# Optimization experiments

Hardware: AMD Instinct MI355X
Metric: run time of the kernel (lower is better)

## Reference

```python
import jax, jax.numpy as jnp
import numpy as np

B, ENC_IN, ENC_HID, N, GH = 64, 64, 256, 2048, 128
LN_EPS = 1e-5


def _chain_adjacency(n):
    # tridiagonal chain adjacency, D^{-1/2} A D^{-1/2} normalized
    off = jnp.ones((n - 1,), dtype=jnp.float32)
    A = jnp.diag(off, 1) + jnp.diag(off, -1)
    deg = A.sum(axis=1)
    d_inv_sqrt = jnp.power(deg + 1e-8, -0.5)
    return A * d_inv_sqrt[None, :] * d_inv_sqrt[:, None]


def setup_inputs() -> dict:
    key = jax.random.key(0)
    ks = jax.random.split(key, 16)
    s = 0.02
    return {
        "x": jax.random.normal(ks[0], (B, ENC_IN), dtype=jnp.float32),
        "A_hat": _chain_adjacency(N),
        "W1": jax.random.normal(ks[1], (ENC_IN, ENC_HID), dtype=jnp.float32) * s,
        "b1": jnp.zeros((ENC_HID,), dtype=jnp.float32),
        "W2": jax.random.normal(ks[2], (ENC_HID, N * GH), dtype=jnp.float32) * s,
        "b2": jnp.zeros((N * GH,), dtype=jnp.float32),
        "Wg1": jax.random.normal(ks[3], (GH, GH), dtype=jnp.float32) * s,
        "Wg2": jax.random.normal(ks[4], (GH, GH), dtype=jnp.float32) * s,
        "ln_g1": jnp.ones((GH,), dtype=jnp.float32),
        "ln_b1": jnp.zeros((GH,), dtype=jnp.float32),
        "ln_g2": jnp.ones((GH,), dtype=jnp.float32),
        "ln_b2": jnp.zeros((GH,), dtype=jnp.float32),
        "Wout": jax.random.normal(ks[5], (GH, 1), dtype=jnp.float32) * s,
        "bout": jnp.zeros((1,), dtype=jnp.float32),
    }


def _layernorm(h, g, b):
    mu = h.mean(axis=-1, keepdims=True)
    var = ((h - mu) ** 2).mean(axis=-1, keepdims=True)
    return (h - mu) * jax.lax.rsqrt(var + LN_EPS) * g + b


def reference(x, A_hat, W1, b1, W2, b2, Wg1, Wg2, ln_g1, ln_b1, ln_g2, ln_b2, Wout, bout):
    # encoder MLP -> (B, N, GH) node features
    enc = jax.nn.relu(x @ W1 + b1) @ W2 + b2
    out = enc.reshape(B, N, GH)
    # GCN layers: out = out + A_hat @ (LN(out) W)   (dropout is identity at eval)
    for Wg, g, bb in ((Wg1, ln_g1, ln_b1), (Wg2, ln_g2, ln_b2)):
        h = _layernorm(out, g, bb)
        Wx = h @ Wg                              # (B, N, GH)
        out = out + jnp.einsum('ij,bjd->bid', A_hat, Wx)
    return (out @ Wout + bout).squeeze(-1)       # (B, N)
```

## Files before the change

kernel.cpp:

```cpp
#include <hip/hip_runtime.h>


#define B_    64
#define EIN   64
#define EHID  256
#define NN    2048
#define GH    128
#define NG    (NN*GH)
#define LN_EPS 1e-5f
#define C3    28

typedef _Float16 f16;
typedef _Float16 f16x8 __attribute__((ext_vector_type(8)));
typedef _Float16 f16x4 __attribute__((ext_vector_type(4)));
typedef _Float16 f16x2 __attribute__((ext_vector_type(2)));
typedef float    f32x4 __attribute__((ext_vector_type(4)));
typedef unsigned int u32;

#define AS1 __attribute__((address_space(1)))
#define AS3 __attribute__((address_space(3)))

__device__ __forceinline__ float wred64(float v) {
#pragma unroll
    for (int off = 32; off > 0; off >>= 1) v += __shfl_xor(v, off, 64);
    return v;
}

__global__ __launch_bounds__(256) void k_prep(
    const float* __restrict__ x,  const float* __restrict__ W1, const float* __restrict__ b1,
    const float* __restrict__ Wg1,const float* __restrict__ Wg2,const float* __restrict__ Wout,
    const float* __restrict__ A_hat,
    const float* __restrict__ ln_g2, const float* __restrict__ ln_b2,
    f16* __restrict__ h1h, f16* __restrict__ wg1T,
    float* __restrict__ u2, float* __restrict__ sc,
    float* __restrict__ clo, float* __restrict__ chi)
{
    int bid = blockIdx.x, tid = threadIdx.x;
    if (bid < 64) {
        int b = bid, j = tid;
        float acc = b1[j];
#pragma unroll 8
        for (int k = 0; k < EIN; ++k) acc = fmaf(x[b*EIN + k], W1[k*EHID + j], acc);
        h1h[b*EHID + j] = (f16)fmaxf(acc, 0.f);
    } else if (bid == 64) {
        __shared__ float tu[GH], tb[GH];
        if (tid < GH) {
            float s = 0.f;
            for (int j = 0; j < GH; ++j) s = fmaf(Wg2[tid*GH + j], Wout[j], s);
            float uu = ln_g2[tid] * s;
            u2[tid] = uu;
            tu[tid] = uu;
            tb[tid] = ln_b2[tid] * s;
        }
        __syncthreads();
        if (tid < 64) {
            float a = tu[tid] + tu[tid + 64];
            float b = tb[tid] + tb[tid + 64];
            a = wred64(a); b = wred64(b);
            if (tid == 0) { sc[0] = a; sc[1] = b; }
        }
    } else if (bid == 65) {
        for (int i = tid; i < GH*GH; i += 256) {
            int n = i >> 7, k = i & 127;
            wg1T[i] = (f16)Wg1[k*GH + n];
        }
    } else {
        int n = (bid - 66) * 256 + tid;
        clo[n] = (n >= 1)    ? A_hat[(size_t)n*NN + (n-1)] : 0.f;
        chi[n] = (n <= NN-2) ? A_hat[(size_t)n*NN + (n+1)] : 0.f;
    }
}

__global__ __launch_bounds__(256) void k_enc(
    const float* __restrict__ W2, const float* __restrict__ b2,
    const f16* __restrict__ h1h, f16* __restrict__ out0)
{
    __shared__ float w2s[2][16*516];

    int tid = threadIdx.x;
    int L = tid & 63, wv = tid >> 6, hi = L >> 4, lo = L & 15;
    int c0 = blockIdx.x * 256;

    auto stage = [&](int kk, int nb) {
#pragma unroll
        for (int s = 0; s < 8; ++s) {
            int r = wv*8 + s;
            const float* gp = W2 + (size_t)(kk*32 + r) * NG + c0 + L*4;
            float* ldst = &w2s[nb][(r >> 1)*516 + (r & 1)*256];
            __builtin_amdgcn_global_load_lds((const AS1 void*)gp, (AS3 void*)ldst, 16, 0, 0);
        }
    };

    f16x8 afq[2][4];
    auto load_af = [&](int kk, int pb) {
#pragma unroll
        for (int bg = 0; bg < 4; ++bg)
            afq[pb][bg] = *(const f16x8*)(h1h + ((bg*16 + lo) << 8) + kk*32 + hi*8);
    };

    load_af(0, 0);
    asm volatile("" ::: "memory");
    stage(0, 0);
    stage(1, 1);

    f32x4 acc[4][4];
#pragma unroll
    for (int bg = 0; bg < 4; ++bg)
#pragma unroll
        for (int t = 0; t < 4; ++t) acc[bg][t] = f32x4{0.f, 0.f, 0.f, 0.f};

#pragma unroll
    for (int kk = 0; kk < 8; ++kk) {
        if (kk < 7) asm volatile("s_waitcnt vmcnt(8)" ::: "memory");
        else        asm volatile("s_waitcnt vmcnt(0)" ::: "memory");
        __builtin_amdgcn_s_barrier();
        asm volatile("" ::: "memory");

        if (kk < 7) load_af(kk + 1, (kk + 1) & 1);

        const float* wb = w2s[kk & 1];
        f16x8 bf[4];
#pragma unroll
        for (int t = 0; t < 4; ++t)
#pragma unroll
            for (int j = 0; j < 8; ++j) {
                int row = hi*8 + j;
                bf[t][j] = (f16)wb[(row >> 1)*516 + (row & 1)*256 + wv*64 + t*16 + lo];
            }

#pragma unroll
        for (int bg = 0; bg < 4; ++bg)
#pragma unroll
            for (int t = 0; t < 4; ++t)
                acc[bg][t] = __builtin_amdgcn_mfma_f32_16x16x32_f16(afq[kk & 1][bg], bf[t], acc[bg][t], 0, 0, 0);

        asm volatile("" ::: "memory");
        __builtin_amdgcn_s_barrier();
        asm volatile("" ::: "memory");
        if (kk < 6) stage(kk + 2, kk & 1);
    }

    float bv[4];
#pragma unroll
    for (int t = 0; t < 4; ++t) bv[t] = b2[c0 + wv*64 + t*16 + lo];
#pragma unroll
    for (int bg = 0; bg < 4; ++bg)
#pragma unroll
        for (int t = 0; t < 4; ++t)
#pragma unroll
            for (int r = 0; r < 4; ++r) {
                int brow = bg*16 + hi*4 + r;
                out0[(size_t)brow * NG + c0 + wv*64 + t*16 + lo] = (f16)(acc[bg][t][r] + bv[t]);
            }
}

__global__ __launch_bounds__(256) void k_gcn(
    const float* __restrict__ clo, const float* __restrict__ chi,
    const float* __restrict__ ln_g1, const float* __restrict__ ln_b1,
    const float* __restrict__ Wout, const float* __restrict__ bout,
    const float* __restrict__ u2, const float* __restrict__ sc,
    const f16* __restrict__ wg1T,
    const f16* __restrict__ out0, float* __restrict__ y)
{
    __shared__ f16 out0_s[32][136];
    __shared__ f16 h0s[32][136];
    __shared__ f16 wx0_s[32][136];
    __shared__ alignas(16) float g1s[GH], b1s[GH], u2s[GH], wos[GH];
    __shared__ float cls[32], chs[32];
    __shared__ float ss[32], yrs[32], scs[2];

    int tid = threadIdx.x;
    int n0 = blockIdx.x * C3;
    int b  = blockIdx.y;

    for (int i = tid; i < 32*16; i += 256) {
        int r = i >> 4, gv = i & 15;
        int n = n0 - 2 + r;
        f16x8 v = {0,0,0,0,0,0,0,0};
        if (n >= 0 && n < NN) v = *(const f16x8*)(out0 + ((size_t)b*NN + n)*GH + gv*8);
        *(f16x8*)&out0_s[r][gv*8] = v;
    }
    if (tid < GH) {
        g1s[tid] = ln_g1[tid]; b1s[tid] = ln_b1[tid];
        u2s[tid] = u2[tid];    wos[tid] = Wout[tid];
    } else if (tid < GH + 32) {
        int r = tid - GH, n = n0 - 2 + r;
        bool ok = (n >= 0 && n < NN);
        cls[r] = ok ? clo[n] : 0.f;
        chs[r] = ok ? chi[n] : 0.f;
    } else if (tid == GH + 32) {
        scs[0] = sc[0]; scs[1] = sc[1];
    }
    __syncthreads();

    int L = tid & 63, wv = tid >> 6, hi = L >> 4, lo = L & 15;

    {
        f32x4 g1a = *(const f32x4*)&g1s[lo*8],     b1a = *(const f32x4*)&b1s[lo*8];
        f32x4 g1b = *(const f32x4*)&g1s[lo*8 + 4], b1b = *(const f32x4*)&b1s[lo*8 + 4];
#pragma unroll
        for (int p = 0; p < 2; ++p) {
            int r = wv*4 + hi + p*16;
            f16x8 xv = *(const f16x8*)&out0_s[r][lo*8];
            float xf[8];
#pragma unroll
            for (int c2 = 0; c2 < 8; ++c2) xf[c2] = (float)xv[c2];
            float s = 0.f, qq = 0.f;
#pragma unroll
            for (int c2 = 0; c2 < 8; ++c2) { s += xf[c2]; qq += xf[c2]*xf[c2]; }
#pragma unroll
            for (int off = 8; off > 0; off >>= 1) {
                s  += __shfl_xor(s,  off, 64);
                qq += __shfl_xor(qq, off, 64);
            }
            float mu  = s * (1.f/128.f);
            float inv = rsqrtf(qq*(1.f/128.f) - mu*mu + LN_EPS);
            f16x8 h;
            h[0] = (f16)((xf[0] - mu)*inv*g1a[0] + b1a[0]);
            h[1] = (f16)((xf[1] - mu)*inv*g1a[1] + b1a[1]);
            h[2] = (f16)((xf[2] - mu)*inv*g1a[2] + b1a[2]);
            h[3] = (f16)((xf[3] - mu)*inv*g1a[3] + b1a[3]);
            h[4] = (f16)((xf[4] - mu)*inv*g1b[0] + b1b[0]);
            h[5] = (f16)((xf[5] - mu)*inv*g1b[1] + b1b[1]);
            h[6] = (f16)((xf[6] - mu)*inv*g1b[2] + b1b[2]);
            h[7] = (f16)((xf[7] - mu)*inv*g1b[3] + b1b[3]);
            *(f16x8*)&h0s[r][lo*8] = h;
        }
    }
    __syncthreads();

    f32x4 acc[2][2];
#pragma unroll
    for (int mg = 0; mg < 2; ++mg)
#pragma unroll
        for (int nt = 0; nt < 2; ++nt) acc[mg][nt] = f32x4{0.f, 0.f, 0.f, 0.f};

#pragma unroll
    for (int kk = 0; kk < 4; ++kk) {
        f16x8 af[2], bfr[2];
#pragma unroll
        for (int mg = 0; mg < 2; ++mg)
            af[mg] = *(const f16x8*)&h0s[mg*16 + lo][kk*32 + hi*8];
#pragma unroll
        for (int nt = 0; nt < 2; ++nt) {
            int n = wv*32 + nt*16 + lo;
            bfr[nt] = *(const f16x8*)(wg1T + n*GH + kk*32 + hi*8);
        }
#pragma unroll
        for (int mg = 0; mg < 2; ++mg)
#pragma unroll
            for (int nt = 0; nt < 2; ++nt)
                acc[mg][nt] = __builtin_amdgcn_mfma_f32_16x16x32_f16(af[mg], bfr[nt], acc[mg][nt], 0, 0, 0);
    }
#pragma unroll
    for (int mg = 0; mg < 2; ++mg)
#pragma unroll
        for (int nt = 0; nt < 2; ++nt)
#pragma unroll
            for (int r = 0; r < 4; ++r)
                wx0_s[mg*16 + hi*4 + r][wv*32 + nt*16 + lo] = (f16)acc[mg][nt][r];
    __syncthreads();

    {
        f32x4 u2a = *(const f32x4*)&u2s[lo*8],     woa = *(const f32x4*)&wos[lo*8];
        f32x4 u2b = *(const f32x4*)&u2s[lo*8 + 4], wob = *(const f32x4*)&wos[lo*8 + 4];
        float S1v = scs[0], S0v = scs[1];
#pragma unroll
        for (int p = 0; p < 2; ++p) {
            int r  = wv*4 + hi + p*16;
            int rm = (r >= 1)  ? r - 1 : 0;
            int rp = (r <= 30) ? r + 1 : 31;
            float c_lo = cls[r], c_hi = chs[r];
            f16x8 ov = *(const f16x8*)&out0_s[r][lo*8];
            f16x8 av = *(const f16x8*)&wx0_s[rm][lo*8];
            f16x8 cv = *(const f16x8*)&wx0_s[rp][lo*8];
            float s = 0.f, qq = 0.f, d = 0.f, yp = 0.f;
#pragma unroll
            for (int c2 = 0; c2 < 8; ++c2) {
                float xx = (float)ov[c2] + c_lo*(float)av[c2] + c_hi*(float)cv[c2];
                float uc = (c2 < 4) ? u2a[c2] : u2b[c2-4];
                float wc = (c2 < 4) ? woa[c2] : wob[c2-4];
                s += xx; qq += xx*xx; d += xx*uc; yp += xx*wc;
            }
#pragma unroll
            for (int off = 8; off > 0; off >>= 1) {
                s  += __shfl_xor(s,  off, 64);
                qq += __shfl_xor(qq, off, 64);
                d  += __shfl_xor(d,  off, 64);
                yp += __shfl_xor(yp, off, 64);
            }
            if (lo == 0 && r >= 1 && r <= 30) {
                float mu  = s * (1.f/128.f);
                float inv = rsqrtf(qq*(1.f/128.f) - mu*mu + LN_EPS);
                ss[r]  = inv*(d - mu*S1v) + S0v;
                yrs[r] = yp;
            }
        }
    }
    __syncthreads();

    if (tid < C3) {
        int n = n0 + tid;
        if (n < NN) {
            int r = tid + 2;
            y[(size_t)b*NN + n] = yrs[r] + bout[0] + cls[r]*ss[r-1] + chs[r]*ss[r+1];
        }
    }
}

extern "C" void kernel_launch(void* const* d_in, const int* in_sizes, int n_in,
                              void* d_out, int out_size, void* d_ws, size_t ws_size,
                              hipStream_t stream)
{
    (void)in_sizes; (void)n_in; (void)out_size; (void)ws_size;
    const float* x    = (const float*)d_in[0];
    const float* A_hat= (const float*)d_in[1];
    const float* W1   = (const float*)d_in[2];
    const float* b1   = (const float*)d_in[3];
    const float* W2   = (const float*)d_in[4];
    const float* b2   = (const float*)d_in[5];
    const float* Wg1  = (const float*)d_in[6];
    const float* Wg2  = (const float*)d_in[7];
    const float* g1   = (const float*)d_in[8];
    const float* lb1  = (const float*)d_in[9];
    const float* g2   = (const float*)d_in[10];
    const float* lb2  = (const float*)d_in[11];
    const float* Wout = (const float*)d_in[12];
    const float* bout = (const float*)d_in[13];
    float* y = (float*)d_out;

    char* ws = (char*)d_ws;
    f16*   h1h  = (f16*)(ws + 0);
    f16*   wg1T = (f16*)(ws + 32768);
    float* u2   = (float*)(ws + 65536);
    float* sc   = (float*)(ws + 66560);
    float* clo  = (float*)(ws + 81920);
    float* chi  = (float*)(ws + 90112);
    f16*   out0 = (f16*)(ws + (1u << 20));

    k_prep<<<dim3(74),                   256, 0, stream>>>(x, W1, b1, Wg1, Wg2, Wout, A_hat,
                                                           g2, lb2,
                                                           h1h, wg1T, u2, sc, clo, chi);
    k_enc <<<dim3(NG/256),               256, 0, stream>>>(W2, b2, h1h, out0);
    k_gcn <<<dim3((NN + C3 - 1)/C3, B_), 256, 0, stream>>>(clo, chi, g1, lb1,
                                                           Wout, bout, u2, sc, wg1T, out0, y);
}
```

Baseline: 440.1 us.

## Keep GCN rows in registers, share one LDS tile, simplify W2 GEMM pipeline

```diff
diff --git a/kernel.cpp b/kernel.cpp
--- a/kernel.cpp
+++ b/kernel.cpp
@@ -91,17 +91,7 @@
         }
     };
 
-    f16x8 afq[2][4];
-    auto load_af = [&](int kk, int pb) {
-#pragma unroll
-        for (int bg = 0; bg < 4; ++bg)
-            afq[pb][bg] = *(const f16x8*)(h1h + ((bg*16 + lo) << 8) + kk*32 + hi*8);
-    };
-
-    load_af(0, 0);
-    asm volatile("" ::: "memory");
     stage(0, 0);
-    stage(1, 1);
 
     f32x4 acc[4][4];
 #pragma unroll
@@ -111,12 +101,8 @@
 
 #pragma unroll
     for (int kk = 0; kk < 8; ++kk) {
-        if (kk < 7) asm volatile("s_waitcnt vmcnt(8)" ::: "memory");
-        else        asm volatile("s_waitcnt vmcnt(0)" ::: "memory");
-        __builtin_amdgcn_s_barrier();
-        asm volatile("" ::: "memory");
-
-        if (kk < 7) load_af(kk + 1, (kk + 1) & 1);
+        __syncthreads();
+        if (kk < 7) stage(kk + 1, (kk + 1) & 1);
 
         const float* wb = w2s[kk & 1];
         f16x8 bf[4];
@@ -128,16 +114,16 @@
                 bf[t][j] = (f16)wb[(row >> 1)*516 + (row & 1)*256 + wv*64 + t*16 + lo];
             }
 
+        f16x8 af[4];
 #pragma unroll
         for (int bg = 0; bg < 4; ++bg)
+            af[bg] = *(const f16x8*)(h1h + ((bg*16 + lo) << 8) + kk*32 + hi*8);
+
+#pragma unroll
+        for (int bg = 0; bg < 4; ++bg)
 #pragma unroll
             for (int t = 0; t < 4; ++t)
-                acc[bg][t] = __builtin_amdgcn_mfma_f32_16x16x32_f16(afq[kk & 1][bg], bf[t], acc[bg][t], 0, 0, 0);
-
-        asm volatile("" ::: "memory");
-        __builtin_amdgcn_s_barrier();
-        asm volatile("" ::: "memory");
-        if (kk < 6) stage(kk + 2, kk & 1);
+                acc[bg][t] = __builtin_amdgcn_mfma_f32_16x16x32_f16(af[bg], bf[t], acc[bg][t], 0, 0, 0);
     }
 
     float bv[4];
@@ -162,9 +148,7 @@
     const f16* __restrict__ wg1T,
     const f16* __restrict__ out0, float* __restrict__ y)
 {
-    __shared__ f16 out0_s[32][136];
-    __shared__ f16 h0s[32][136];
-    __shared__ f16 wx0_s[32][136];
+    __shared__ f16 hw_s[32][136];
     __shared__ alignas(16) float g1s[GH], b1s[GH], u2s[GH], wos[GH];
     __shared__ float cls[32], chs[32];
     __shared__ float ss[32], yrs[32], scs[2];
@@ -172,14 +156,19 @@
     int tid = threadIdx.x;
     int n0 = blockIdx.x * C3;
     int b  = blockIdx.y;
-
-    for (int i = tid; i < 32*16; i += 256) {
-        int r = i >> 4, gv = i & 15;
+    int L = tid & 63, wv = tid >> 6, hi = L >> 4, lo = L & 15;
+
+    float xf[2][8];
+#pragma unroll
+    for (int p = 0; p < 2; ++p) {
+        int r = wv*4 + hi + p*16;
         int n = n0 - 2 + r;
         f16x8 v = {0,0,0,0,0,0,0,0};
-        if (n >= 0 && n < NN) v = *(const f16x8*)(out0 + ((size_t)b*NN + n)*GH + gv*8);
-        *(f16x8*)&out0_s[r][gv*8] = v;
-    }
+        if (n >= 0 && n < NN) v = *(const f16x8*)(out0 + ((size_t)b*NN + n)*GH + lo*8);
+#pragma unroll
+        for (int c2 = 0; c2 < 8; ++c2) xf[p][c2] = (float)v[c2];
+    }
+
     if (tid < GH) {
         g1s[tid] = ln_g1[tid]; b1s[tid] = ln_b1[tid];
         u2s[tid] = u2[tid];    wos[tid] = Wout[tid];
@@ -191,9 +180,22 @@
     } else if (tid == GH + 32) {
         scs[0] = sc[0]; scs[1] = sc[1];
     }
-    __syncthreads();
-
-    int L = tid & 63, wv = tid >> 6, hi = L >> 4, lo = L & 15;
+
+    float mu[2], inv[2];
+#pragma unroll
+    for (int p = 0; p < 2; ++p) {
+        float s = 0.f, qq = 0.f;
+#pragma unroll
+        for (int c2 = 0; c2 < 8; ++c2) { s += xf[p][c2]; qq += xf[p][c2]*xf[p][c2]; }
+#pragma unroll
+        for (int off = 8; off > 0; off >>= 1) {
+            s  += __shfl_xor(s,  off, 64);
+            qq += __shfl_xor(qq, off, 64);
+        }
+        mu[p]  = s * (1.f/128.f);
+        inv[p] = rsqrtf(qq*(1.f/128.f) - mu[p]*mu[p] + LN_EPS);
+    }
+    __syncthreads();
 
     {
         f32x4 g1a = *(const f32x4*)&g1s[lo*8],     b1a = *(const f32x4*)&b1s[lo*8];
@@ -201,30 +203,16 @@
 #pragma unroll
         for (int p = 0; p < 2; ++p) {
             int r = wv*4 + hi + p*16;
-            f16x8 xv = *(const f16x8*)&out0_s[r][lo*8];
-            float xf[8];
-#pragma unroll
-            for (int c2 = 0; c2 < 8; ++c2) xf[c2] = (float)xv[c2];
-            float s = 0.f, qq = 0.f;
-#pragma unroll
-            for (int c2 = 0; c2 < 8; ++c2) { s += xf[c2]; qq += xf[c2]*xf[c2]; }
-#pragma unroll
-            for (int off = 8; off > 0; off >>= 1) {
-                s  += __shfl_xor(s,  off, 64);
-                qq += __shfl_xor(qq, off, 64);
-            }
-            float mu  = s * (1.f/128.f);
-            float inv = rsqrtf(qq*(1.f/128.f) - mu*mu + LN_EPS);
             f16x8 h;
-            h[0] = (f16)((xf[0] - mu)*inv*g1a[0] + b1a[0]);
-            h[1] = (f16)((xf[1] - mu)*inv*g1a[1] + b1a[1]);
-            h[2] = (f16)((xf[2] - mu)*inv*g1a[2] + b1a[2]);
-            h[3] = (f16)((xf[3] - mu)*inv*g1a[3] + b1a[3]);
-            h[4] = (f16)((xf[4] - mu)*inv*g1b[0] + b1b[0]);
-            h[5] = (f16)((xf[5] - mu)*inv*g1b[1] + b1b[1]);
-            h[6] = (f16)((xf[6] - mu)*inv*g1b[2] + b1b[2]);
-            h[7] = (f16)((xf[7] - mu)*inv*g1b[3] + b1b[3]);
-            *(f16x8*)&h0s[r][lo*8] = h;
+            h[0] = (f16)((xf[p][0] - mu[p])*inv[p]*g1a[0] + b1a[0]);
+            h[1] = (f16)((xf[p][1] - mu[p])*inv[p]*g1a[1] + b1a[1]);
+            h[2] = (f16)((xf[p][2] - mu[p])*inv[p]*g1a[2] + b1a[2]);
+            h[3] = (f16)((xf[p][3] - mu[p])*inv[p]*g1a[3] + b1a[3]);
+            h[4] = (f16)((xf[p][4] - mu[p])*inv[p]*g1b[0] + b1b[0]);
+            h[5] = (f16)((xf[p][5] - mu[p])*inv[p]*g1b[1] + b1b[1]);
+            h[6] = (f16)((xf[p][6] - mu[p])*inv[p]*g1b[2] + b1b[2]);
+            h[7] = (f16)((xf[p][7] - mu[p])*inv[p]*g1b[3] + b1b[3]);
+            *(f16x8*)&hw_s[r][lo*8] = h;
         }
     }
     __syncthreads();
@@ -240,7 +228,7 @@
         f16x8 af[2], bfr[2];
 #pragma unroll
         for (int mg = 0; mg < 2; ++mg)
-            af[mg] = *(const f16x8*)&h0s[mg*16 + lo][kk*32 + hi*8];
+            af[mg] = *(const f16x8*)&hw_s[mg*16 + lo][kk*32 + hi*8];
 #pragma unroll
         for (int nt = 0; nt < 2; ++nt) {
             int n = wv*32 + nt*16 + lo;
@@ -252,13 +240,14 @@
             for (int nt = 0; nt < 2; ++nt)
                 acc[mg][nt] = __builtin_amdgcn_mfma_f32_16x16x32_f16(af[mg], bfr[nt], acc[mg][nt], 0, 0, 0);
     }
+    __syncthreads();
 #pragma unroll
     for (int mg = 0; mg < 2; ++mg)
 #pragma unroll
         for (int nt = 0; nt < 2; ++nt)
 #pragma unroll
             for (int r = 0; r < 4; ++r)
-                wx0_s[mg*16 + hi*4 + r][wv*32 + nt*16 + lo] = (f16)acc[mg][nt][r];
+                hw_s[mg*16 + hi*4 + r][wv*32 + nt*16 + lo] = (f16)acc[mg][nt][r];
     __syncthreads();
 
     {
@@ -271,13 +260,12 @@
             int rm = (r >= 1)  ? r - 1 : 0;
             int rp = (r <= 30) ? r + 1 : 31;
             float c_lo = cls[r], c_hi = chs[r];
-            f16x8 ov = *(const f16x8*)&out0_s[r][lo*8];
-            f16x8 av = *(const f16x8*)&wx0_s[rm][lo*8];
-            f16x8 cv = *(const f16x8*)&wx0_s[rp][lo*8];
+            f16x8 av = *(const f16x8*)&hw_s[rm][lo*8];
+            f16x8 cv = *(const f16x8*)&hw_s[rp][lo*8];
             float s = 0.f, qq = 0.f, d = 0.f, yp = 0.f;
 #pragma unroll
             for (int c2 = 0; c2 < 8; ++c2) {
-                float xx = (float)ov[c2] + c_lo*(float)av[c2] + c_hi*(float)cv[c2];
+                float xx = xf[p][c2] + c_lo*(float)av[c2] + c_hi*(float)cv[c2];
                 float uc = (c2 < 4) ? u2a[c2] : u2b[c2-4];
                 float wc = (c2 < 4) ? woa[c2] : wob[c2-4];
                 s += xx; qq += xx*xx; d += xx*uc; yp += xx*wc;
@@ -290,9 +278,9 @@
                 yp += __shfl_xor(yp, off, 64);
             }
             if (lo == 0 && r >= 1 && r <= 30) {
-                float mu  = s * (1.f/128.f);
-                float inv = rsqrtf(qq*(1.f/128.f) - mu*mu + LN_EPS);
-                ss[r]  = inv*(d - mu*S1v) + S0v;
+                float muv  = s * (1.f/128.f);
+                float invv = rsqrtf(qq*(1.f/128.f) - muv*muv + LN_EPS);
+                ss[r]  = invv*(d - muv*S1v) + S0v;
                 yrs[r] = yp;
             }
         }
```

After: 435.9 us. About the same (-1.0%).
